# Optimization experiments

Measured on AMD Instinct MI355X. Metric: run time of the kernel, lower is better.

## Reference

```python
import jax, jax.numpy as jnp
import numpy as np

B, D, N, H = 8, 256, 2048, 4  # batch, d_model, seq_len, heads
HEAD_DIM = D // H


def _proj(x, W, b):
    # Conv1D(kernel_size=1) applied to (b, n, d) == dense over channels.
    # x: (B, D, N); W: (D, D) [in, out]; b: (D,) -> (B, D, N)
    return jnp.einsum('bdn,do->bon', x, W) + b[None, :, None]


def setup_inputs() -> dict:
    key = jax.random.key(0)
    ks = jax.random.split(key, 11)
    s = 0.02
    inp = {
        'query': jax.random.normal(ks[0], (B, D, N), jnp.float32),
        'key':   jax.random.normal(ks[1], (B, D, N), jnp.float32),
        'value': jax.random.normal(ks[2], (B, D, N), jnp.float32),
        'Wq': jax.random.normal(ks[3], (D, D), jnp.float32) * s,
        'bq': jnp.zeros((D,), jnp.float32),
        'Wk': jax.random.normal(ks[4], (D, D), jnp.float32) * s,
        'bk': jnp.zeros((D,), jnp.float32),
        'Wv': jax.random.normal(ks[5], (D, D), jnp.float32) * s,
        'bv': jnp.zeros((D,), jnp.float32),
        'Wm': jax.random.normal(ks[6], (D, D), jnp.float32) * s,
        'bm': jnp.zeros((D,), jnp.float32),
    }
    return inp


def reference(query, key, value, Wq, bq, Wk, bk, Wv, bv, Wm, bm):
    b = query.shape[0]
    # project and split heads: (B, D, N) -> (B, head_dim, H, N)
    # NOTE: TF reshape splits d_model as (head_dim, heads) with head_dim outer.
    q = _proj(query, Wq, bq).reshape(b, HEAD_DIM, H, N)
    k = _proj(key,   Wk, bk).reshape(b, HEAD_DIM, H, N)
    v = _proj(value, Wv, bv).reshape(b, HEAD_DIM, H, N)
    # attention with scale 1/sqrt(head_dim)
    scores = jnp.einsum('bdhn,bdhm->bhnm', q, k) / jnp.sqrt(jnp.asarray(HEAD_DIM, q.dtype))
    prob = jax.nn.softmax(scores, axis=-1)
    x = jnp.einsum('bhnm,bdhm->bdhn', prob, v)  # (B, head_dim, H, N)
    x = x.reshape(b, D, N)
    return _proj(x, Wm, bm)
```

## Files before the change

### kernel.cpp

```cpp
#include <hip/hip_runtime.h>
#include <stdint.h>

#define BB 8
#define DD 256
#define NN 2048
#define HH 4
#define HD 64
#define SCALE_Q 0.18033688011112042f

typedef __attribute__((ext_vector_type(8))) short bf16x8;
typedef __attribute__((ext_vector_type(4))) float f32x4;
typedef __attribute__((ext_vector_type(16))) float f32x16;


__device__ __forceinline__ void gld16(const void* g, void* l) {
  __builtin_amdgcn_global_load_lds(
      (__attribute__((address_space(1))) void*)(void*)(uintptr_t)(g),
      (__attribute__((address_space(3))) void*)(l), 16, 0, 0);
}

__device__ __forceinline__ unsigned short f2bf(float f) {
  union { float f; unsigned u; } v; v.f = f;
  unsigned lsb = (v.u >> 16) & 1u;
  v.u += 0x7fffu + lsb;
  return (unsigned short)(v.u >> 16);
}


__global__ __launch_bounds__(256) void tcast_x(
    const float* __restrict__ q, const float* __restrict__ k,
    const float* __restrict__ v, unsigned short* __restrict__ oq,
    unsigned short* __restrict__ ok2, unsigned short* __restrict__ ov) {
  __shared__ float t[32][33];
  int z = blockIdx.z, src = z >> 3, b = z & 7;
  const float* ip = (src == 0 ? q : src == 1 ? k : v) + (long)b * DD * NN;
  unsigned short* op = (src == 0 ? oq : src == 1 ? ok2 : ov) + (long)b * NN * DD;
  int c0 = blockIdx.x * 32, r0 = blockIdx.y * 32;
  int tx = threadIdx.x & 31, ty = threadIdx.x >> 5;
#pragma unroll
  for (int rr = 0; rr < 4; rr++) {
    int r = rr * 8 + ty;
    t[r][tx] = ip[(long)(r0 + r) * NN + c0 + tx];
  }
  __syncthreads();
#pragma unroll
  for (int rr = 0; rr < 4; rr++) {
    int c = rr * 8 + ty;
    op[(long)(c0 + c) * DD + r0 + tx] = f2bf(t[tx][c]);
  }
}


__global__ __launch_bounds__(256) void tcast_w(
    const float* __restrict__ Wq, const float* __restrict__ Wk,
    const float* __restrict__ Wv, const float* __restrict__ Wm,
    unsigned short* __restrict__ oWq, unsigned short* __restrict__ oWk,
    unsigned short* __restrict__ oWv, unsigned short* __restrict__ oWm) {
  __shared__ float t[32][33];
  int z = blockIdx.z;
  const float* ip = z == 0 ? Wq : z == 1 ? Wk : z == 2 ? Wv : Wm;
  unsigned short* op = z == 0 ? oWq : z == 1 ? oWk : z == 2 ? oWv : oWm;
  float s = z == 0 ? SCALE_Q : 1.f;
  int c0 = blockIdx.x * 32, r0 = blockIdx.y * 32;
  int tx = threadIdx.x & 31, ty = threadIdx.x >> 5;
#pragma unroll
  for (int rr = 0; rr < 4; rr++) {
    int r = rr * 8 + ty;
    t[r][tx] = ip[(long)(r0 + r) * DD + c0 + tx];
  }
  __syncthreads();
  if (z < 3) {
#pragma unroll
    for (int rr = 0; rr < 4; rr++) {
      int c = rr * 8 + ty;
      int o = c0 + c;
      int jp = ((o & 3) << 6) | (o >> 2);
      op[(long)jp * DD + r0 + tx] = f2bf(s * t[tx][c]);
    }
  } else {
#pragma unroll
    for (int rr = 0; rr < 4; rr++) {
      int c = rr * 8 + ty;
      int d = r0 + tx;
      int kp = ((d & 3) << 6) | (d >> 2);
      op[(long)(c0 + c) * DD + kp] = f2bf(t[tx][c]);
    }
  }
}


__global__ __launch_bounds__(256) void gemm_qkv(
    const unsigned short* __restrict__ Xq, const unsigned short* __restrict__ Xk,
    const unsigned short* __restrict__ Xv, const unsigned short* __restrict__ Wq,
    const unsigned short* __restrict__ Wk, const unsigned short* __restrict__ Wv,
    const float* __restrict__ bq, const float* __restrict__ bk,
    const float* __restrict__ bv, unsigned short* __restrict__ Qh,
    unsigned short* __restrict__ Kh, unsigned short* __restrict__ Vh) {
  constexpr int K = DD;
  __shared__ unsigned short At[128 * 64], Bt[128 * 64];
  int z = blockIdx.z, proj = z >> 3, bb = z & 7;
  const unsigned short *A, *Bp;
  const float* bias;
  float bsc = 1.f;
  int i0, j0;
  if (proj == 0) {
    A = Xq + (long)bb * NN * DD; Bp = Wq; bias = bq; bsc = SCALE_Q;
    i0 = blockIdx.x * 128; j0 = blockIdx.y * 128;
  } else if (proj == 1) {
    A = Xk + (long)bb * NN * DD; Bp = Wk; bias = bk;
    i0 = blockIdx.x * 128; j0 = blockIdx.y * 128;
  } else {
    A = Wv; Bp = Xv + (long)bb * NN * DD; bias = bv;
    i0 = blockIdx.y * 128; j0 = blockIdx.x * 128;
  }
  int tid = threadIdx.x, lane = tid & 63, w = tid >> 6;
  int wr = w >> 1, wc = w & 1;

  f32x4 acc[4][4];
#pragma unroll
  for (int a = 0; a < 4; a++)
#pragma unroll
    for (int c = 0; c < 4; c++) acc[a][c] = (f32x4){0.f, 0.f, 0.f, 0.f};

  for (int kt = 0; kt < 4; kt++) {
    if (kt) __syncthreads();
#pragma unroll
    for (int c = 0; c < 4; c++) {
      int row = w * 32 + c * 8 + (lane >> 3);
      int so = ((lane & 7) * 16) ^ ((row & 7) << 4);
      gld16((const char*)A + ((long)(i0 + row) * K + kt * 64) * 2 + so,
            (char*)At + (w * 32 + c * 8) * 128);
      gld16((const char*)Bp + ((long)(j0 + row) * K + kt * 64) * 2 + so,
            (char*)Bt + (w * 32 + c * 8) * 128);
    }
    __syncthreads();
#pragma unroll
    for (int ks = 0; ks < 2; ks++) {
      bf16x8 af[4], bfv[4];
#pragma unroll
      for (int mi = 0; mi < 4; mi++) {
        int row = wr * 64 + mi * 16 + (lane & 15);
        int off = (ks * 64 + (lane >> 4) * 16) ^ ((row & 7) << 4);
        af[mi] = *(const bf16x8*)((const char*)At + row * 128 + off);
      }
#pragma unroll
      for (int nj = 0; nj < 4; nj++) {
        int row = wc * 64 + nj * 16 + (lane & 15);
        int off = (ks * 64 + (lane >> 4) * 16) ^ ((row & 7) << 4);
        bfv[nj] = *(const bf16x8*)((const char*)Bt + row * 128 + off);
      }
#pragma unroll
      for (int mi = 0; mi < 4; mi++)
#pragma unroll
        for (int nj = 0; nj < 4; nj++)
          acc[mi][nj] = __builtin_amdgcn_mfma_f32_16x16x32_bf16(
              af[mi], bfv[nj], acc[mi][nj], 0, 0, 0);
    }
  }

#pragma unroll
  for (int mi = 0; mi < 4; mi++) {
#pragma unroll
    for (int nj = 0; nj < 4; nj++) {
#pragma unroll
      for (int r = 0; r < 4; r++) {
        int ig = i0 + wr * 64 + mi * 16 + (lane >> 4) * 4 + r;
        int jg = j0 + wc * 64 + nj * 16 + (lane & 15);
        float v = acc[mi][nj][r];
        if (proj < 2) {
          int o = ((jg & 63) << 2) | (jg >> 6);
          v += bias[o] * bsc;
          int hh = jg >> 6, hd = jg & 63;
          unsigned short* dst = proj == 0 ? Qh : Kh;
          dst[(((long)bb * HH + hh) * NN + ig) * HD + hd] = f2bf(v);
        } else {
          int o = ((ig & 63) << 2) | (ig >> 6);
          v += bias[o];
          int hh = ig >> 6, hd = ig & 63;
          Vh[(((long)bb * HH + hh) * HD + hd) * NN + jg] = f2bf(v);
        }
      }
    }
  }
}


__global__ __launch_bounds__(256) void attn_kernel(
    const unsigned short* __restrict__ Q, const unsigned short* __restrict__ Kg,
    const unsigned short* __restrict__ V, unsigned short* __restrict__ XA) {
  __shared__ unsigned short Kt[2][64 * 64];
  __shared__ unsigned short Vt[2][64 * 64];
  int h = blockIdx.y, b = blockIdx.z;
  int tid = threadIdx.x, lane = tid & 63, w = tid >> 6;
  int l31 = lane & 31, hi = lane >> 5;
  int q0 = blockIdx.x * 128 + w * 32;
  long hb = (long)b * HH + h;
  const unsigned short* Qb = Q + hb * NN * HD;
  const unsigned short* Kb = Kg + hb * NN * HD;
  const unsigned short* Vb = V + hb * HD * NN;

  bf16x8 qf[4];
#pragma unroll
  for (int ks = 0; ks < 4; ks++)
    qf[ks] = *(const bf16x8*)(Qb + (long)(q0 + l31) * HD + ks * 16 + hi * 8);

  f32x16 oA[2];
#pragma unroll
  for (int hf = 0; hf < 2; hf++)
#pragma unroll
    for (int r = 0; r < 16; r++) oA[hf][r] = 0.f;
  float lsum = 0.f;

  auto stage = [&](int buf, int t) {
    int m0 = t * 64;
#pragma unroll
    for (int c = 0; c < 2; c++) {
      int row = w * 16 + c * 8 + (lane >> 3);
      int so = ((lane & 7) * 16) ^ ((row & 7) << 4);
      gld16((const char*)Kb + (long)(m0 + row) * 128 + so,
            (char*)&Kt[buf][0] + (w * 16 + c * 8) * 128);
      gld16((const char*)Vb + ((long)row * NN + m0) * 2 + so,
            (char*)&Vt[buf][0] + (w * 16 + c * 8) * 128);
    }
  };

  int cur = 0;
  stage(0, 0);
  __syncthreads();

  for (int t = 0; t < NN / 64; t++) {
    if (t + 1 < NN / 64) stage(cur ^ 1, t + 1);

#pragma unroll
    for (int kh = 0; kh < 2; kh++) {
      f32x16 s;
#pragma unroll
      for (int r = 0; r < 16; r++) s[r] = 0.f;
#pragma unroll
      for (int ks = 0; ks < 4; ks++) {
        int row = kh * 32 + l31;
        int off = (ks * 32 + hi * 16) ^ ((row & 7) << 4);
        bf16x8 kf = *(const bf16x8*)((const char*)&Kt[cur][0] + row * 128 + off);
        s = __builtin_amdgcn_mfma_f32_32x32x16_bf16(kf, qf[ks], s, 0, 0, 0);
      }
      float p[16];
#pragma unroll
      for (int r = 0; r < 16; r++) {
        p[r] = __builtin_amdgcn_exp2f(s[r]);
        lsum += p[r];
      }
      unsigned pk[8];
#pragma unroll
      for (int i = 0; i < 8; i++)
        asm("v_cvt_pk_bf16_f32 %0, %1, %2"
            : "=v"(pk[i]) : "v"(p[2 * i]), "v"(p[2 * i + 1]));
      asm volatile("v_permlane32_swap_b32 %0, %1" : "+v"(pk[0]), "+v"(pk[2]));
      asm volatile("v_permlane32_swap_b32 %0, %1" : "+v"(pk[1]), "+v"(pk[3]));
      asm volatile("v_permlane32_swap_b32 %0, %1" : "+v"(pk[4]), "+v"(pk[6]));
      asm volatile("v_permlane32_swap_b32 %0, %1" : "+v"(pk[5]), "+v"(pk[7]));
#pragma unroll
      for (int sv = 0; sv < 2; sv++) {
        union { bf16x8 v; unsigned u[4]; } fr;
        fr.u[0] = pk[sv * 4 + 0]; fr.u[1] = pk[sv * 4 + 1];
        fr.u[2] = pk[sv * 4 + 2]; fr.u[3] = pk[sv * 4 + 3];
#pragma unroll
        for (int hf = 0; hf < 2; hf++) {
          int vrow = hf * 32 + l31;
          int voff = ((2 * kh + sv) * 32 + hi * 16) ^ ((vrow & 7) << 4);
          bf16x8 vf = *(const bf16x8*)((const char*)&Vt[cur][0] + vrow * 128 + voff);
          oA[hf] = __builtin_amdgcn_mfma_f32_32x32x16_bf16(fr.v, vf, oA[hf], 0, 0, 0);
        }
      }
    }
    __syncthreads();
    cur ^= 1;
  }

  float lt = lsum + __shfl_xor(lsum, 32);
#pragma unroll
  for (int r = 0; r < 16; r++) {
    int qrow = (r & 3) + 8 * (r >> 2) + 4 * hi;
    float linv = 1.0f / __shfl(lt, qrow);
    long nrow = (long)b * NN + q0 + qrow;
#pragma unroll
    for (int hf = 0; hf < 2; hf++) {
      float val = oA[hf][r] * linv;
      XA[nrow * DD + h * HD + hf * 32 + l31] = f2bf(val);
    }
  }
}


__global__ __launch_bounds__(256) void gemm_out(
    const unsigned short* __restrict__ A, const unsigned short* __restrict__ B,
    const float* __restrict__ bias, float* __restrict__ out) {
  constexpr int K = DD;
  __shared__ unsigned short At[128 * 64], Bt[128 * 64];
  int bb = blockIdx.z;
  const unsigned short* Ab = A;
  const unsigned short* Bb = B + (long)bb * NN * DD;
  int i0 = blockIdx.x * 128, j0 = blockIdx.y * 128;
  int tid = threadIdx.x, lane = tid & 63, w = tid >> 6;
  int wr = w >> 1, wc = w & 1;

  f32x4 acc[4][4];
#pragma unroll
  for (int a = 0; a < 4; a++)
#pragma unroll
    for (int c = 0; c < 4; c++) acc[a][c] = (f32x4){0.f, 0.f, 0.f, 0.f};

  for (int kt = 0; kt < 4; kt++) {
    if (kt) __syncthreads();
#pragma unroll
    for (int c = 0; c < 4; c++) {
      int row = w * 32 + c * 8 + (lane >> 3);
      int so = ((lane & 7) * 16) ^ ((row & 7) << 4);
      gld16((const char*)Ab + ((long)(i0 + row) * K + kt * 64) * 2 + so,
            (char*)At + (w * 32 + c * 8) * 128);
      gld16((const char*)Bb + ((long)(j0 + row) * K + kt * 64) * 2 + so,
            (char*)Bt + (w * 32 + c * 8) * 128);
    }
    __syncthreads();
#pragma unroll
    for (int ks = 0; ks < 2; ks++) {
      bf16x8 af[4], bfv[4];
#pragma unroll
      for (int mi = 0; mi < 4; mi++) {
        int row = wr * 64 + mi * 16 + (lane & 15);
        int off = (ks * 64 + (lane >> 4) * 16) ^ ((row & 7) << 4);
        af[mi] = *(const bf16x8*)((const char*)At + row * 128 + off);
      }
#pragma unroll
      for (int nj = 0; nj < 4; nj++) {
        int row = wc * 64 + nj * 16 + (lane & 15);
        int off = (ks * 64 + (lane >> 4) * 16) ^ ((row & 7) << 4);
        bfv[nj] = *(const bf16x8*)((const char*)Bt + row * 128 + off);
      }
#pragma unroll
      for (int mi = 0; mi < 4; mi++)
#pragma unroll
        for (int nj = 0; nj < 4; nj++)
          acc[mi][nj] = __builtin_amdgcn_mfma_f32_16x16x32_bf16(
              af[mi], bfv[nj], acc[mi][nj], 0, 0, 0);
    }
  }

#pragma unroll
  for (int mi = 0; mi < 4; mi++) {
#pragma unroll
    for (int nj = 0; nj < 4; nj++) {
#pragma unroll
      for (int r = 0; r < 4; r++) {
        int ig = i0 + wr * 64 + mi * 16 + (lane >> 4) * 4 + r;
        int jg = j0 + wc * 64 + nj * 16 + (lane & 15);
        out[((long)bb * DD + ig) * NN + jg] = acc[mi][nj][r] + bias[ig];
      }
    }
  }
}


extern "C" void kernel_launch(void* const* d_in, const int* in_sizes, int n_in,
                              void* d_out, int out_size, void* d_ws, size_t ws_size,
                              hipStream_t stream) {
  const float* q_in = (const float*)d_in[0];
  const float* k_in = (const float*)d_in[1];
  const float* v_in = (const float*)d_in[2];
  const float* Wq = (const float*)d_in[3];
  const float* bq = (const float*)d_in[4];
  const float* Wk = (const float*)d_in[5];
  const float* bk = (const float*)d_in[6];
  const float* Wv = (const float*)d_in[7];
  const float* bv = (const float*)d_in[8];
  const float* Wm = (const float*)d_in[9];
  const float* bm = (const float*)d_in[10];
  float* out = (float*)d_out;

  const long SX = (long)BB * NN * DD;
  const long SW = (long)DD * DD;
  unsigned short* Xqt = (unsigned short*)d_ws;
  unsigned short* Xkt = Xqt + SX;
  unsigned short* Xvt = Xkt + SX;
  unsigned short* Qh = Xvt + SX;
  unsigned short* Kh = Qh + SX;
  unsigned short* Vh = Kh + SX;
  unsigned short* Wqt = Vh + SX;
  unsigned short* Wkt = Wqt + SW;
  unsigned short* Wvt = Wkt + SW;
  unsigned short* Wmt = Wvt + SW;
  unsigned short* XAt = Xqt;
  if (ws_size < (size_t)(6 * SX + 4 * SW) * 2) return;

  dim3 blk(256);
  tcast_x<<<dim3(NN / 32, DD / 32, 24), blk, 0, stream>>>(
      q_in, k_in, v_in, Xqt, Xkt, Xvt);
  tcast_w<<<dim3(DD / 32, DD / 32, 4), blk, 0, stream>>>(
      Wq, Wk, Wv, Wm, Wqt, Wkt, Wvt, Wmt);
  gemm_qkv<<<dim3(NN / 128, DD / 128, 24), blk, 0, stream>>>(
      Xqt, Xkt, Xvt, Wqt, Wkt, Wvt, bq, bk, bv, Qh, Kh, Vh);
  attn_kernel<<<dim3(NN / 128, HH, BB), blk, 0, stream>>>(Qh, Kh, Vh, XAt);
  gemm_out<<<dim3(DD / 128, NN / 128, BB), blk, 0, stream>>>(Wmt, XAt, bm, out);
}
```

Measured before the change: 197.4 us.

## Double-buffer GEMMs with smaller tiles, register-load K in attention, larger transpose tiles

The QKV and output GEMMs now use 128x64 tiles with double-buffered LDS staging, which doubles the block count and overlaps global loads with MFMA work. The attention kernel loads K fragments straight from global memory into registers, ping-ponging between two register sets, and keeps only V in LDS. MFMA sections are wrapped in s_setprio. The input transpose-cast kernel moves to 64x64 tiles. In exchange, attention uses more registers (which may lower occupancy) and K reads are no longer shared through LDS.

```diff
diff --git a/kernel.cpp b/kernel.cpp
--- a/kernel.cpp
+++ b/kernel.cpp
@@ -31,21 +31,21 @@
     const float* __restrict__ q, const float* __restrict__ k,
     const float* __restrict__ v, unsigned short* __restrict__ oq,
     unsigned short* __restrict__ ok2, unsigned short* __restrict__ ov) {
-  __shared__ float t[32][33];
+  __shared__ float t[64][65];
   int z = blockIdx.z, src = z >> 3, b = z & 7;
   const float* ip = (src == 0 ? q : src == 1 ? k : v) + (long)b * DD * NN;
   unsigned short* op = (src == 0 ? oq : src == 1 ? ok2 : ov) + (long)b * NN * DD;
-  int c0 = blockIdx.x * 32, r0 = blockIdx.y * 32;
-  int tx = threadIdx.x & 31, ty = threadIdx.x >> 5;
-#pragma unroll
-  for (int rr = 0; rr < 4; rr++) {
-    int r = rr * 8 + ty;
+  int c0 = blockIdx.x * 64, r0 = blockIdx.y * 64;
+  int tx = threadIdx.x & 63, ty = threadIdx.x >> 6;
+#pragma unroll
+  for (int rr = 0; rr < 16; rr++) {
+    int r = rr * 4 + ty;
     t[r][tx] = ip[(long)(r0 + r) * NN + c0 + tx];
   }
   __syncthreads();
 #pragma unroll
-  for (int rr = 0; rr < 4; rr++) {
-    int c = rr * 8 + ty;
+  for (int rr = 0; rr < 16; rr++) {
+    int c = rr * 4 + ty;
     op[(long)(c0 + c) * DD + r0 + tx] = f2bf(t[tx][c]);
   }
 }
@@ -89,6 +89,58 @@
 }
 
 
+#define GEMM_STAGE(kt, buf)                                                    \
+  {                                                                            \
+    int _kt = (kt);                                                            \
+    _Pragma("unroll") for (int c = 0; c < 4; c++) {                            \
+      int row = w * 32 + c * 8 + (lane >> 3);                                  \
+      int so = ((lane & 7) * 16) ^ ((row & 7) << 4);                           \
+      gld16((const char*)Ag + ((long)(i0 + row) * DD + _kt * 64) * 2 + so,     \
+            (char*)&At[buf][0] + (w * 32 + c * 8) * 128);                      \
+    }                                                                          \
+    _Pragma("unroll") for (int c = 0; c < 2; c++) {                            \
+      int row = w * 16 + c * 8 + (lane >> 3);                                  \
+      int so = ((lane & 7) * 16) ^ ((row & 7) << 4);                           \
+      gld16((const char*)Bg + ((long)(j0 + row) * DD + _kt * 64) * 2 + so,     \
+            (char*)&Bt[buf][0] + (w * 16 + c * 8) * 128);                      \
+    }                                                                          \
+  }
+
+#define GEMM_COMPUTE(buf)                                                      \
+  _Pragma("unroll") for (int ks = 0; ks < 2; ks++) {                           \
+    bf16x8 af[4], bfv[2];                                                      \
+    _Pragma("unroll") for (int mi = 0; mi < 4; mi++) {                         \
+      int row = wr * 64 + mi * 16 + (lane & 15);                               \
+      int off = (ks * 64 + (lane >> 4) * 16) ^ ((row & 7) << 4);               \
+      af[mi] = *(const bf16x8*)((const char*)&At[buf][0] + row * 128 + off);   \
+    }                                                                          \
+    _Pragma("unroll") for (int nj = 0; nj < 2; nj++) {                         \
+      int row = wc * 32 + nj * 16 + (lane & 15);                               \
+      int off = (ks * 64 + (lane >> 4) * 16) ^ ((row & 7) << 4);               \
+      bfv[nj] = *(const bf16x8*)((const char*)&Bt[buf][0] + row * 128 + off);  \
+    }                                                                          \
+    _Pragma("unroll") for (int mi = 0; mi < 4; mi++)                           \
+        _Pragma("unroll") for (int nj = 0; nj < 2; nj++)                       \
+            acc[mi][nj] = __builtin_amdgcn_mfma_f32_16x16x32_bf16(             \
+                af[mi], bfv[nj], acc[mi][nj], 0, 0, 0);                        \
+  }
+
+#define GEMM_MAIN()                                                            \
+  f32x4 acc[4][2];                                                             \
+  _Pragma("unroll") for (int a = 0; a < 4; a++)                                \
+      _Pragma("unroll") for (int c = 0; c < 2; c++)                            \
+          acc[a][c] = (f32x4){0.f, 0.f, 0.f, 0.f};                             \
+  GEMM_STAGE(0, 0);                                                            \
+  __syncthreads();                                                             \
+  int buf = 0;                                                                 \
+  for (int kt = 0; kt < 4; kt++) {                                             \
+    if (kt < 3) GEMM_STAGE(kt + 1, buf ^ 1);                                   \
+    GEMM_COMPUTE(buf);                                                         \
+    __syncthreads();                                                           \
+    buf ^= 1;                                                                  \
+  }
+
+
 __global__ __launch_bounds__(256) void gemm_qkv(
     const unsigned short* __restrict__ Xq, const unsigned short* __restrict__ Xk,
     const unsigned short* __restrict__ Xv, const unsigned short* __restrict__ Wq,
@@ -96,76 +148,36 @@
     const float* __restrict__ bq, const float* __restrict__ bk,
     const float* __restrict__ bv, unsigned short* __restrict__ Qh,
     unsigned short* __restrict__ Kh, unsigned short* __restrict__ Vh) {
-  constexpr int K = DD;
-  __shared__ unsigned short At[128 * 64], Bt[128 * 64];
+  __shared__ unsigned short At[2][128 * 64], Bt[2][64 * 64];
   int z = blockIdx.z, proj = z >> 3, bb = z & 7;
-  const unsigned short *A, *Bp;
+  int flat = blockIdx.y * 16 + blockIdx.x;
+  const unsigned short *Ag, *Bg;
   const float* bias;
   float bsc = 1.f;
   int i0, j0;
   if (proj == 0) {
-    A = Xq + (long)bb * NN * DD; Bp = Wq; bias = bq; bsc = SCALE_Q;
-    i0 = blockIdx.x * 128; j0 = blockIdx.y * 128;
+    Ag = Xq + (long)bb * NN * DD; Bg = Wq; bias = bq; bsc = SCALE_Q;
+    i0 = (flat & 15) * 128; j0 = (flat >> 4) * 64;
   } else if (proj == 1) {
-    A = Xk + (long)bb * NN * DD; Bp = Wk; bias = bk;
-    i0 = blockIdx.x * 128; j0 = blockIdx.y * 128;
+    Ag = Xk + (long)bb * NN * DD; Bg = Wk; bias = bk;
+    i0 = (flat & 15) * 128; j0 = (flat >> 4) * 64;
   } else {
-    A = Wv; Bp = Xv + (long)bb * NN * DD; bias = bv;
-    i0 = blockIdx.y * 128; j0 = blockIdx.x * 128;
+    Ag = Wv; Bg = Xv + (long)bb * NN * DD; bias = bv;
+    i0 = (flat >> 5) * 128; j0 = (flat & 31) * 64;
   }
   int tid = threadIdx.x, lane = tid & 63, w = tid >> 6;
   int wr = w >> 1, wc = w & 1;
 
-  f32x4 acc[4][4];
-#pragma unroll
-  for (int a = 0; a < 4; a++)
-#pragma unroll
-    for (int c = 0; c < 4; c++) acc[a][c] = (f32x4){0.f, 0.f, 0.f, 0.f};
-
-  for (int kt = 0; kt < 4; kt++) {
-    if (kt) __syncthreads();
-#pragma unroll
-    for (int c = 0; c < 4; c++) {
-      int row = w * 32 + c * 8 + (lane >> 3);
-      int so = ((lane & 7) * 16) ^ ((row & 7) << 4);
-      gld16((const char*)A + ((long)(i0 + row) * K + kt * 64) * 2 + so,
-            (char*)At + (w * 32 + c * 8) * 128);
-      gld16((const char*)Bp + ((long)(j0 + row) * K + kt * 64) * 2 + so,
-            (char*)Bt + (w * 32 + c * 8) * 128);
-    }
-    __syncthreads();
-#pragma unroll
-    for (int ks = 0; ks < 2; ks++) {
-      bf16x8 af[4], bfv[4];
-#pragma unroll
-      for (int mi = 0; mi < 4; mi++) {
-        int row = wr * 64 + mi * 16 + (lane & 15);
-        int off = (ks * 64 + (lane >> 4) * 16) ^ ((row & 7) << 4);
-        af[mi] = *(const bf16x8*)((const char*)At + row * 128 + off);
-      }
-#pragma unroll
-      for (int nj = 0; nj < 4; nj++) {
-        int row = wc * 64 + nj * 16 + (lane & 15);
-        int off = (ks * 64 + (lane >> 4) * 16) ^ ((row & 7) << 4);
-        bfv[nj] = *(const bf16x8*)((const char*)Bt + row * 128 + off);
-      }
-#pragma unroll
-      for (int mi = 0; mi < 4; mi++)
-#pragma unroll
-        for (int nj = 0; nj < 4; nj++)
-          acc[mi][nj] = __builtin_amdgcn_mfma_f32_16x16x32_bf16(
-              af[mi], bfv[nj], acc[mi][nj], 0, 0, 0);
-    }
-  }
+  GEMM_MAIN();
 
 #pragma unroll
   for (int mi = 0; mi < 4; mi++) {
 #pragma unroll
-    for (int nj = 0; nj < 4; nj++) {
+    for (int nj = 0; nj < 2; nj++) {
 #pragma unroll
       for (int r = 0; r < 4; r++) {
         int ig = i0 + wr * 64 + mi * 16 + (lane >> 4) * 4 + r;
-        int jg = j0 + wc * 64 + nj * 16 + (lane & 15);
+        int jg = j0 + wc * 32 + nj * 16 + (lane & 15);
         float v = acc[mi][nj][r];
         if (proj < 2) {
           int o = ((jg & 63) << 2) | (jg >> 6);
@@ -185,10 +197,38 @@
 }
 
 
+__global__ __launch_bounds__(256) void gemm_out(
+    const unsigned short* __restrict__ A, const unsigned short* __restrict__ B,
+    const float* __restrict__ bias, float* __restrict__ out) {
+  __shared__ unsigned short At[2][128 * 64], Bt[2][64 * 64];
+  int bb = blockIdx.z;
+  int flat = blockIdx.y * 16 + blockIdx.x;
+  const unsigned short* Ag = A;
+  const unsigned short* Bg = B + (long)bb * NN * DD;
+  int i0 = (flat >> 5) * 128, j0 = (flat & 31) * 64;
+  int tid = threadIdx.x, lane = tid & 63, w = tid >> 6;
+  int wr = w >> 1, wc = w & 1;
+
+  GEMM_MAIN();
+
+#pragma unroll
+  for (int mi = 0; mi < 4; mi++) {
+#pragma unroll
+    for (int nj = 0; nj < 2; nj++) {
+#pragma unroll
+      for (int r = 0; r < 4; r++) {
+        int ig = i0 + wr * 64 + mi * 16 + (lane >> 4) * 4 + r;
+        int jg = j0 + wc * 32 + nj * 16 + (lane & 15);
+        out[((long)bb * DD + ig) * NN + jg] = acc[mi][nj][r] + bias[ig];
+      }
+    }
+  }
+}
+
+
 __global__ __launch_bounds__(256) void attn_kernel(
     const unsigned short* __restrict__ Q, const unsigned short* __restrict__ Kg,
     const unsigned short* __restrict__ V, unsigned short* __restrict__ XA) {
-  __shared__ unsigned short Kt[2][64 * 64];
   __shared__ unsigned short Vt[2][64 * 64];
   int h = blockIdx.y, b = blockIdx.z;
   int tid = threadIdx.x, lane = tid & 63, w = tid >> 6;
@@ -211,38 +251,36 @@
     for (int r = 0; r < 16; r++) oA[hf][r] = 0.f;
   float lsum = 0.f;
 
-  auto stage = [&](int buf, int t) {
+  auto stageV = [&](int vbuf, int t) {
     int m0 = t * 64;
 #pragma unroll
     for (int c = 0; c < 2; c++) {
       int row = w * 16 + c * 8 + (lane >> 3);
       int so = ((lane & 7) * 16) ^ ((row & 7) << 4);
-      gld16((const char*)Kb + (long)(m0 + row) * 128 + so,
-            (char*)&Kt[buf][0] + (w * 16 + c * 8) * 128);
       gld16((const char*)Vb + ((long)row * NN + m0) * 2 + so,
-            (char*)&Vt[buf][0] + (w * 16 + c * 8) * 128);
+            (char*)&Vt[vbuf][0] + (w * 16 + c * 8) * 128);
     }
   };
-
-  int cur = 0;
-  stage(0, 0);
-  __syncthreads();
-
-  for (int t = 0; t < NN / 64; t++) {
-    if (t + 1 < NN / 64) stage(cur ^ 1, t + 1);
-
+  auto loadK = [&](bf16x8 (&kf)[8], int t) {
+    int m0 = t * 64;
+#pragma unroll
+    for (int kh = 0; kh < 2; kh++)
+#pragma unroll
+      for (int ks = 0; ks < 4; ks++)
+        kf[kh * 4 + ks] =
+            *(const bf16x8*)(Kb + (long)(m0 + kh * 32 + l31) * HD + ks * 16 + hi * 8);
+  };
+  auto body = [&](const bf16x8 (&kf)[8], int vbuf) {
 #pragma unroll
     for (int kh = 0; kh < 2; kh++) {
       f32x16 s;
 #pragma unroll
       for (int r = 0; r < 16; r++) s[r] = 0.f;
-#pragma unroll
-      for (int ks = 0; ks < 4; ks++) {
-        int row = kh * 32 + l31;
-        int off = (ks * 32 + hi * 16) ^ ((row & 7) << 4);
-        bf16x8 kf = *(const bf16x8*)((const char*)&Kt[cur][0] + row * 128 + off);
-        s = __builtin_amdgcn_mfma_f32_32x32x16_bf16(kf, qf[ks], s, 0, 0, 0);
-      }
+      __builtin_amdgcn_s_setprio(1);
+#pragma unroll
+      for (int ks = 0; ks < 4; ks++)
+        s = __builtin_amdgcn_mfma_f32_32x32x16_bf16(kf[kh * 4 + ks], qf[ks], s, 0, 0, 0);
+      __builtin_amdgcn_s_setprio(0);
       float p[16];
 #pragma unroll
       for (int r = 0; r < 16; r++) {
@@ -263,17 +301,35 @@
         union { bf16x8 v; unsigned u[4]; } fr;
         fr.u[0] = pk[sv * 4 + 0]; fr.u[1] = pk[sv * 4 + 1];
         fr.u[2] = pk[sv * 4 + 2]; fr.u[3] = pk[sv * 4 + 3];
+        __builtin_amdgcn_s_setprio(1);
 #pragma unroll
         for (int hf = 0; hf < 2; hf++) {
           int vrow = hf * 32 + l31;
           int voff = ((2 * kh + sv) * 32 + hi * 16) ^ ((vrow & 7) << 4);
-          bf16x8 vf = *(const bf16x8*)((const char*)&Vt[cur][0] + vrow * 128 + voff);
+          bf16x8 vf = *(const bf16x8*)((const char*)&Vt[vbuf][0] + vrow * 128 + voff);
           oA[hf] = __builtin_amdgcn_mfma_f32_32x32x16_bf16(fr.v, vf, oA[hf], 0, 0, 0);
         }
+        __builtin_amdgcn_s_setprio(0);
       }
     }
+  };
+
+  bf16x8 kfA[8], kfB[8];
+  loadK(kfA, 0);
+  stageV(0, 0);
+  __syncthreads();
+
+  for (int t = 0; t < NN / 64; t += 2) {
+    stageV(1, t + 1);
+    loadK(kfB, t + 1);
+    body(kfA, 0);
     __syncthreads();
-    cur ^= 1;
+    if (t + 2 < NN / 64) {
+      stageV(0, t + 2);
+      loadK(kfA, t + 2);
+    }
+    body(kfB, 1);
+    __syncthreads();
   }
 
   float lt = lsum + __shfl_xor(lsum, 32);
@@ -286,75 +342,6 @@
     for (int hf = 0; hf < 2; hf++) {
       float val = oA[hf][r] * linv;
       XA[nrow * DD + h * HD + hf * 32 + l31] = f2bf(val);
-    }
-  }
-}
-
-
-__global__ __launch_bounds__(256) void gemm_out(
-    const unsigned short* __restrict__ A, const unsigned short* __restrict__ B,
-    const float* __restrict__ bias, float* __restrict__ out) {
-  constexpr int K = DD;
-  __shared__ unsigned short At[128 * 64], Bt[128 * 64];
-  int bb = blockIdx.z;
-  const unsigned short* Ab = A;
-  const unsigned short* Bb = B + (long)bb * NN * DD;
-  int i0 = blockIdx.x * 128, j0 = blockIdx.y * 128;
-  int tid = threadIdx.x, lane = tid & 63, w = tid >> 6;
-  int wr = w >> 1, wc = w & 1;
-
-  f32x4 acc[4][4];
-#pragma unroll
-  for (int a = 0; a < 4; a++)
-#pragma unroll
-    for (int c = 0; c < 4; c++) acc[a][c] = (f32x4){0.f, 0.f, 0.f, 0.f};
-
-  for (int kt = 0; kt < 4; kt++) {
-    if (kt) __syncthreads();
-#pragma unroll
-    for (int c = 0; c < 4; c++) {
-      int row = w * 32 + c * 8 + (lane >> 3);
-      int so = ((lane & 7) * 16) ^ ((row & 7) << 4);
-      gld16((const char*)Ab + ((long)(i0 + row) * K + kt * 64) * 2 + so,
-            (char*)At + (w * 32 + c * 8) * 128);
-      gld16((const char*)Bb + ((long)(j0 + row) * K + kt * 64) * 2 + so,
-            (char*)Bt + (w * 32 + c * 8) * 128);
-    }
-    __syncthreads();
-#pragma unroll
-    for (int ks = 0; ks < 2; ks++) {
-      bf16x8 af[4], bfv[4];
-#pragma unroll
-      for (int mi = 0; mi < 4; mi++) {
-        int row = wr * 64 + mi * 16 + (lane & 15);
-        int off = (ks * 64 + (lane >> 4) * 16) ^ ((row & 7) << 4);
-        af[mi] = *(const bf16x8*)((const char*)At + row * 128 + off);
-      }
-#pragma unroll
-      for (int nj = 0; nj < 4; nj++) {
-        int row = wc * 64 + nj * 16 + (lane & 15);
-        int off = (ks * 64 + (lane >> 4) * 16) ^ ((row & 7) << 4);
-        bfv[nj] = *(const bf16x8*)((const char*)Bt + row * 128 + off);
-      }
-#pragma unroll
-      for (int mi = 0; mi < 4; mi++)
-#pragma unroll
-        for (int nj = 0; nj < 4; nj++)
-          acc[mi][nj] = __builtin_amdgcn_mfma_f32_16x16x32_bf16(
-              af[mi], bfv[nj], acc[mi][nj], 0, 0, 0);
-    }
-  }
-
-#pragma unroll
-  for (int mi = 0; mi < 4; mi++) {
-#pragma unroll
-    for (int nj = 0; nj < 4; nj++) {
-#pragma unroll
-      for (int r = 0; r < 4; r++) {
-        int ig = i0 + wr * 64 + mi * 16 + (lane >> 4) * 4 + r;
-        int jg = j0 + wc * 64 + nj * 16 + (lane & 15);
-        out[((long)bb * DD + ig) * NN + jg] = acc[mi][nj][r] + bias[ig];
-      }
     }
   }
 }
@@ -392,12 +379,12 @@
   if (ws_size < (size_t)(6 * SX + 4 * SW) * 2) return;
 
   dim3 blk(256);
-  tcast_x<<<dim3(NN / 32, DD / 32, 24), blk, 0, stream>>>(
+  tcast_x<<<dim3(NN / 64, DD / 64, 24), blk, 0, stream>>>(
       q_in, k_in, v_in, Xqt, Xkt, Xvt);
   tcast_w<<<dim3(DD / 32, DD / 32, 4), blk, 0, stream>>>(
       Wq, Wk, Wv, Wm, Wqt, Wkt, Wvt, Wmt);
-  gemm_qkv<<<dim3(NN / 128, DD / 128, 24), blk, 0, stream>>>(
+  gemm_qkv<<<dim3(16, 4, 24), blk, 0, stream>>>(
       Xqt, Xkt, Xvt, Wqt, Wkt, Wvt, bq, bk, bv, Qh, Kh, Vh);
   attn_kernel<<<dim3(NN / 128, HH, BB), blk, 0, stream>>>(Qh, Kh, Vh, XAt);
-  gemm_out<<<dim3(DD / 128, NN / 128, BB), blk, 0, stream>>>(Wmt, XAt, bm, out);
-}
+  gemm_out<<<dim3(16, 4, 8), blk, 0, stream>>>(Wmt, XAt, bm, out);
+}
```

Result: slower. 215.8 us (+9.4%).
